# Optimization experiments

Measured on AMD Instinct MI355X. Metric: run time of the kernel, lower is better.

The kernel has to match this reference:

```python
import jax, jax.numpy as jnp
import numpy as np

H = 2048  # hidden_size
I = 2048  # input_size
B = 2048  # batch


def setup_inputs() -> dict:
    key = jax.random.key(0)
    k0, k1, k2, k3, k4, k5 = jax.random.split(key, 6)
    # bipolar-domain activations live in [-1, 1]
    inp = jax.random.uniform(k0, (B, I), jnp.float32, minval=-1.0, maxval=1.0)
    hx = jax.random.uniform(k1, (B, H), jnp.float32, minval=-1.0, maxval=1.0)
    s = 1.0 / np.sqrt(H + I)
    w_f = jax.random.normal(k2, (H, H + I), jnp.float32) * s
    b_f = jax.random.normal(k3, (H,), jnp.float32) * s
    w_n = jax.random.normal(k4, (H, H + I), jnp.float32) * s
    b_n = jax.random.normal(k5, (H,), jnp.float32) * s
    return {"input": inp, "hx": hx, "w_f": w_f, "b_f": b_f, "w_n": w_n, "b_n": b_n}


def reference(input, hx, w_f, b_f, w_n, b_n):
    # Expected-value (probability-domain) math of the unary bitstream MGU cell.
    # fg_ug_tanh: FSULinear on [hx, x]; 'hardtanh is direct pass' -> identity act.
    fg_ug_in = jnp.concatenate([hx, input], axis=1)            # [B, H+I]
    fg_in = fg_ug_in @ w_f.T + b_f                              # [B, H]
    # fg_sigmoid: FSUAdd of [fg_in, ones] with scale=None -> (x + 1) / 2
    fg = (fg_in + 1.0) * 0.5                                    # [B, H]
    # fg_hx_mul: FSUMul with static in_1_prob = hx buffer
    fg_hx = fg * hx                                             # [B, H]
    # ng_ug_tanh: FSULinear on [fg*hx, x]
    ng_ug_in = jnp.concatenate([fg_hx, input], axis=1)          # [B, H+I]
    ng = ng_ug_in @ w_n.T + b_n                                 # [B, H]
    # fg_ng_mul: dynamic FSUMul; bipolar bit-inversion (1 - bitstream) negates value
    fg_ng = fg * ng
    # hy_add: FSUAdd([ng, -fg*ng, fg*hx], scale=1) -> plain sum
    hy = ng - fg_ng + fg_hx                                     # = (1-fg)*ng + fg*hx
    return hy
```

## Files before the change

### kernel.cpp

```cpp
#include <hip/hip_runtime.h>
#include <stdint.h>


#define Hdim 2048
#define Idim 2048
#define Bdim 2048
#define Ktot 4096
#define KHALF 2048
#define NSTEP (KHALF / 64)

typedef __bf16 bf16;
typedef __bf16 bf16x8 __attribute__((ext_vector_type(8)));
typedef float  f32x4  __attribute__((ext_vector_type(4)));

__device__ __forceinline__ void gload_lds16(const bf16* g, bf16* l) {
  __builtin_amdgcn_global_load_lds(
      (const __attribute__((address_space(1))) unsigned int*)g,
      (__attribute__((address_space(3))) unsigned int*)l,
      16, 0, 0);
}

__global__ void prep_kernel(const float* __restrict__ w_f, const float* __restrict__ w_n,
                            const float* __restrict__ hx, const float* __restrict__ x,
                            bf16* __restrict__ Wf, bf16* __restrict__ Wn,
                            bf16* __restrict__ A1) {
  const int n8 = Hdim * Ktot / 8;
  int stride = gridDim.x * blockDim.x;
  for (int i = blockIdx.x * blockDim.x + threadIdx.x; i < 3 * n8; i += stride) {
    const float* src;
    bf16* dst;
    if (i < n8) {
      src = w_f + (size_t)i * 8;  dst = Wf + (size_t)i * 8;
    } else if (i < 2 * n8) {
      int j = i - n8;
      src = w_n + (size_t)j * 8;  dst = Wn + (size_t)j * 8;
    } else {
      int j = i - 2 * n8;
      int e = j * 8;
      int b = e >> 12;
      int k = e & (Ktot - 1);
      src = (k < Hdim) ? (hx + (size_t)b * Hdim + k)
                       : (x  + (size_t)b * Idim + (k - Hdim));
      dst = A1 + (size_t)e;
    }
    const float4* s = (const float4*)src;
    float4 va = s[0], vb = s[1];
    bf16x8 o;
    o[0]=(bf16)va.x; o[1]=(bf16)va.y; o[2]=(bf16)va.z; o[3]=(bf16)va.w;
    o[4]=(bf16)vb.x; o[5]=(bf16)vb.y; o[6]=(bf16)vb.z; o[7]=(bf16)vb.w;
    *((bf16x8*)dst) = o;
  }
}

template<int EPI>
__global__ __launch_bounds__(512)
void gemm_kernel(const bf16* __restrict__ A1, const bf16* __restrict__ A2L,
                 const bf16* __restrict__ W,
                 const float* __restrict__ bias,
                 const float* __restrict__ hx,
                 bf16* __restrict__ OMF,
                 bf16* __restrict__ A2Lw,
                 float* __restrict__ OUT)
{
  __shared__ bf16 lds[2][2][2][8192];

  int bid  = blockIdx.x;
  int sbid = (bid & 7) * 32 + (bid >> 3);
  int tm = sbid >> 4, tn = sbid & 15;

  int tid  = threadIdx.x;
  int w = tid >> 6, lane = tid & 63;
  int g = w >> 2, sub = w & 3;
  int wrow = (sub >> 1) * 64;
  int wcol = (sub & 1) * 64;
  int fr = lane & 15, fq = lane >> 4;
  int swz = fr & 7;

  int gtid = sub * 64 + lane;
  int srow = gtid >> 3;
  int csrc = (gtid & 7) ^ (srow & 7);

  const bf16* pA;
  size_t strA;
  if (EPI == 0) {
    pA = A1 + (size_t)(tm * 128 + srow) * Ktot + csrc * 8 + g * KHALF;
    strA = Ktot;
  } else if (g == 0) {
    pA = A2L + (size_t)(tm * 128 + srow) * KHALF + csrc * 8;
    strA = KHALF;
  } else {
    pA = A1 + (size_t)(tm * 128 + srow) * Ktot + csrc * 8 + Hdim;
    strA = Ktot;
  }
  const bf16* pB = W + (size_t)(tn * 128 + srow) * Ktot + csrc * 8 + g * KHALF;
  int lbase = sub * 512;

#define STAGE(buf, koff) do {                                                      \
    _Pragma("unroll")                                                              \
    for (int jj = 0; jj < 4; ++jj) {                                               \
      gload_lds16(pA + (size_t)jj * 32 * strA + (koff), &lds[g][buf][0][jj * 2048 + lbase]); \
      gload_lds16(pB + (size_t)jj * 32 * Ktot + (koff), &lds[g][buf][1][jj * 2048 + lbase]); \
    }                                                                              \
  } while (0)

#define READS(buf_, j_) do {                                                       \
    int ch = (((j_) * 4 + fq) ^ swz) * 8;                                          \
    _Pragma("unroll")                                                              \
    for (int m = 0; m < 4; ++m)                                                    \
      af[m] = *(const bf16x8*)&lds[g][buf_][0][(wrow + m * 16 + fr) * 64 + ch];    \
    _Pragma("unroll")                                                              \
    for (int n = 0; n < 4; ++n)                                                    \
      bv[n] = *(const bf16x8*)&lds[g][buf_][1][(wcol + n * 16 + fr) * 64 + ch];    \
  } while (0)

  f32x4 acc[4][4] = {};

  STAGE(0, 0);

  const int NW = 2 * NSTEP + 1;
  for (int win = 0; win < NW; ++win) {
    int w2 = win - g;
    bool active = (unsigned)w2 < (unsigned)(2 * NSTEP);
    int t = w2 >> 1, j = w2 & 1, buf = t & 1;
    bf16x8 af[4], bv[4];
    if (active) {
      if (j == 1) READS(buf, 1);
      else asm volatile("s_waitcnt vmcnt(0)" ::: "memory");
    }
    __builtin_amdgcn_s_barrier();
    if (active) {
      if (j == 0) {
        READS(buf, 0);
        if (t + 1 < NSTEP) STAGE(buf ^ 1, (t + 1) * 64);
      }
      __builtin_amdgcn_s_setprio(1);
      #pragma unroll
      for (int m = 0; m < 4; ++m)
        #pragma unroll
        for (int n = 0; n < 4; ++n)
          acc[m][n] = __builtin_amdgcn_mfma_f32_16x16x32_bf16(af[m], bv[n], acc[m][n], 0, 0, 0);
      __builtin_amdgcn_s_setprio(0);
    }
  }
#undef STAGE
#undef READS

  __syncthreads();
  float* xch = (float*)&lds[0][0][0][0];
  if (g == 1) {
    #pragma unroll
    for (int m = 0; m < 4; ++m)
      #pragma unroll
      for (int n = 0; n < 4; ++n)
        *(f32x4*)&xch[sub * 4096 + (m * 4 + n) * 256 + lane * 4] = acc[m][n];
  }
  __syncthreads();
  if (g == 0) {
    int row0 = tm * 128 + wrow + fq * 4;
    int col0 = tn * 128 + wcol + fr;
    #pragma unroll
    for (int n = 0; n < 4; ++n) {
      int gcol = col0 + n * 16;
      float bv = bias[gcol];
      #pragma unroll
      for (int m = 0; m < 4; ++m) {
        f32x4 part = *(const f32x4*)&xch[sub * 4096 + (m * 4 + n) * 256 + lane * 4];
        #pragma unroll
        for (int i = 0; i < 4; ++i) {
          int grow = row0 + m * 16 + i;
          size_t idx = (size_t)grow * Hdim + gcol;
          float v = acc[m][n][i] + part[i] + bv;
          if (EPI == 0) {
            float fg   = (v + 1.0f) * 0.5f;
            float fghx = fg * hx[idx];
            OMF[idx]  = (bf16)(1.0f - fg);
            A2Lw[(size_t)grow * KHALF + gcol] = (bf16)fghx;
          } else {
            float omf  = (float)OMF[idx];
            float fghx = (float)A2L[idx];
            OUT[idx] = omf * v + fghx;
          }
        }
      }
    }
  }
}

extern "C" void kernel_launch(void* const* d_in, const int* in_sizes, int n_in,
                              void* d_out, int out_size, void* d_ws, size_t ws_size,
                              hipStream_t stream) {
  const float* x   = (const float*)d_in[0];
  const float* hx  = (const float*)d_in[1];
  const float* w_f = (const float*)d_in[2];
  const float* b_f = (const float*)d_in[3];
  const float* w_n = (const float*)d_in[4];
  const float* b_n = (const float*)d_in[5];
  float* out = (float*)d_out;

  bf16* A1  = (bf16*)d_ws;
  bf16* A2L = A1  + (size_t)Bdim * Ktot;
  bf16* Wf  = A2L + (size_t)Bdim * KHALF;
  bf16* Wn  = Wf  + (size_t)Hdim * Ktot;
  bf16* OMF = Wn  + (size_t)Hdim * Ktot;

  prep_kernel<<<2048, 256, 0, stream>>>(w_f, w_n, hx, x, Wf, Wn, A1);

  gemm_kernel<0><<<256, 512, 0, stream>>>(A1, nullptr, Wf, b_f, hx, OMF, A2L, nullptr);
  gemm_kernel<1><<<256, 512, 0, stream>>>(A1, A2L, Wn, b_n, nullptr, OMF, nullptr, out);
}
```

Baseline: 115.9 us.

## Give each wave private LDS tiles with BK=32 and drop workgroup barriers

The GEMM main loop changes from workgroup-shared 128x128 LDS tiles, with barrier-synchronised staggered split-K groups, to per-wave private 64x32 A and B tiles. Each wave now loads its own tiles by direct global-to-LDS copies and waits only on its own vmcnt, so the s_barrier in the loop is gone. The K step drops from 64 to 32 and the XOR swizzle is redone for the narrower rows. The cost is lost cross-wave reuse: each A and B row block is now fetched by two waves, which doubles L2-to-LDS traffic, and the smaller K step adds loop and wait overhead.

```diff
diff --git a/kernel.cpp b/kernel.cpp
--- a/kernel.cpp
+++ b/kernel.cpp
@@ -7,7 +7,8 @@
 #define Bdim 2048
 #define Ktot 4096
 #define KHALF 2048
-#define NSTEP (KHALF / 64)
+#define BK 32
+#define NSTEP (KHALF / BK)
 
 typedef __bf16 bf16;
 typedef __bf16 bf16x8 __attribute__((ext_vector_type(8)));
@@ -62,7 +63,7 @@
                  bf16* __restrict__ A2Lw,
                  float* __restrict__ OUT)
 {
-  __shared__ bf16 lds[2][2][2][8192];
+  __shared__ bf16 lds[8][2][2][64 * BK];
 
   int bid  = blockIdx.x;
   int sbid = (bid & 7) * 32 + (bid >> 3);
@@ -74,76 +75,62 @@
   int wrow = (sub >> 1) * 64;
   int wcol = (sub & 1) * 64;
   int fr = lane & 15, fq = lane >> 4;
-  int swz = fr & 7;
+  int permr = (fr >> 1) & 3;
 
-  int gtid = sub * 64 + lane;
-  int srow = gtid >> 3;
-  int csrc = (gtid & 7) ^ (srow & 7);
+  int srowL   = lane >> 2;
+  int schunkL = (lane & 3) ^ ((lane >> 3) & 3);
 
-  const bf16* pA;
+  const bf16* pAl;
   size_t strA;
   if (EPI == 0) {
-    pA = A1 + (size_t)(tm * 128 + srow) * Ktot + csrc * 8 + g * KHALF;
+    pAl = A1 + (size_t)(tm * 128 + wrow + srowL) * Ktot + schunkL * 8 + g * KHALF;
     strA = Ktot;
   } else if (g == 0) {
-    pA = A2L + (size_t)(tm * 128 + srow) * KHALF + csrc * 8;
+    pAl = A2L + (size_t)(tm * 128 + wrow + srowL) * KHALF + schunkL * 8;
     strA = KHALF;
   } else {
-    pA = A1 + (size_t)(tm * 128 + srow) * Ktot + csrc * 8 + Hdim;
+    pAl = A1 + (size_t)(tm * 128 + wrow + srowL) * Ktot + schunkL * 8 + Hdim;
     strA = Ktot;
   }
-  const bf16* pB = W + (size_t)(tn * 128 + srow) * Ktot + csrc * 8 + g * KHALF;
-  int lbase = sub * 512;
+  const bf16* pBl = W + (size_t)(tn * 128 + wcol + srowL) * Ktot + schunkL * 8 + g * KHALF;
 
-#define STAGE(buf, koff) do {                                                      \
-    _Pragma("unroll")                                                              \
-    for (int jj = 0; jj < 4; ++jj) {                                               \
-      gload_lds16(pA + (size_t)jj * 32 * strA + (koff), &lds[g][buf][0][jj * 2048 + lbase]); \
-      gload_lds16(pB + (size_t)jj * 32 * Ktot + (koff), &lds[g][buf][1][jj * 2048 + lbase]); \
-    }                                                                              \
-  } while (0)
-
-#define READS(buf_, j_) do {                                                       \
-    int ch = (((j_) * 4 + fq) ^ swz) * 8;                                          \
-    _Pragma("unroll")                                                              \
-    for (int m = 0; m < 4; ++m)                                                    \
-      af[m] = *(const bf16x8*)&lds[g][buf_][0][(wrow + m * 16 + fr) * 64 + ch];    \
-    _Pragma("unroll")                                                              \
-    for (int n = 0; n < 4; ++n)                                                    \
-      bv[n] = *(const bf16x8*)&lds[g][buf_][1][(wcol + n * 16 + fr) * 64 + ch];    \
+#define STAGE(buf_, t_) do {                                                   \
+    _Pragma("unroll")                                                          \
+    for (int i = 0; i < 4; ++i) {                                              \
+      gload_lds16(pAl + (size_t)i * 16 * strA + (t_) * BK, &lds[w][buf_][0][i * 512]); \
+      gload_lds16(pBl + (size_t)i * 16 * Ktot + (t_) * BK, &lds[w][buf_][1][i * 512]); \
+    }                                                                          \
   } while (0)
 
   f32x4 acc[4][4] = {};
 
   STAGE(0, 0);
-
-  const int NW = 2 * NSTEP + 1;
-  for (int win = 0; win < NW; ++win) {
-    int w2 = win - g;
-    bool active = (unsigned)w2 < (unsigned)(2 * NSTEP);
-    int t = w2 >> 1, j = w2 & 1, buf = t & 1;
+  int cur = 0;
+  for (int t = 0; t < NSTEP; ++t) {
+    if (t + 1 < NSTEP) {
+      STAGE(cur ^ 1, t + 1);
+      asm volatile("s_waitcnt vmcnt(8)" ::: "memory");
+    } else {
+      asm volatile("s_waitcnt vmcnt(0)" ::: "memory");
+    }
     bf16x8 af[4], bv[4];
-    if (active) {
-      if (j == 1) READS(buf, 1);
-      else asm volatile("s_waitcnt vmcnt(0)" ::: "memory");
-    }
-    __builtin_amdgcn_s_barrier();
-    if (active) {
-      if (j == 0) {
-        READS(buf, 0);
-        if (t + 1 < NSTEP) STAGE(buf ^ 1, (t + 1) * 64);
-      }
-      __builtin_amdgcn_s_setprio(1);
+    int ch = (fq ^ permr) * 8;
+    #pragma unroll
+    for (int m = 0; m < 4; ++m)
+      af[m] = *(const bf16x8*)&lds[w][cur][0][(m * 16 + fr) * BK + ch];
+    #pragma unroll
+    for (int n = 0; n < 4; ++n)
+      bv[n] = *(const bf16x8*)&lds[w][cur][1][(n * 16 + fr) * BK + ch];
+    __builtin_amdgcn_s_setprio(1);
+    #pragma unroll
+    for (int m = 0; m < 4; ++m)
       #pragma unroll
-      for (int m = 0; m < 4; ++m)
-        #pragma unroll
-        for (int n = 0; n < 4; ++n)
-          acc[m][n] = __builtin_amdgcn_mfma_f32_16x16x32_bf16(af[m], bv[n], acc[m][n], 0, 0, 0);
-      __builtin_amdgcn_s_setprio(0);
-    }
+      for (int n = 0; n < 4; ++n)
+        acc[m][n] = __builtin_amdgcn_mfma_f32_16x16x32_bf16(af[m], bv[n], acc[m][n], 0, 0, 0);
+    __builtin_amdgcn_s_setprio(0);
+    cur ^= 1;
   }
 #undef STAGE
-#undef READS
 
   __syncthreads();
   float* xch = (float*)&lds[0][0][0][0];
@@ -161,7 +148,7 @@
     #pragma unroll
     for (int n = 0; n < 4; ++n) {
       int gcol = col0 + n * 16;
-      float bv = bias[gcol];
+      float bv2 = bias[gcol];
       #pragma unroll
       for (int m = 0; m < 4; ++m) {
         f32x4 part = *(const f32x4*)&xch[sub * 4096 + (m * 4 + n) * 256 + lane * 4];
@@ -169,7 +156,7 @@
         for (int i = 0; i < 4; ++i) {
           int grow = row0 + m * 16 + i;
           size_t idx = (size_t)grow * Hdim + gcol;
-          float v = acc[m][n][i] + part[i] + bv;
+          float v = acc[m][n][i] + part[i] + bv2;
           if (EPI == 0) {
             float fg   = (v + 1.0f) * 0.5f;
             float fghx = fg * hx[idx];
```

New measurement: 150.5 us. +29.9%, slower.
